# Kernel tuning notes

Measured on AMD Instinct MI355X. Metric: run time of the kernel, lower is better.

## Reference

```python
import jax, jax.numpy as jnp
import numpy as np

VOCAB = 6; C_IN = 4; D = 256; L = 4; T = 4096; B = 2
EXPAND = 2; DI = EXPAND * D  # 512
DS = 16; DCONV = 4; DTR = 16  # dt_rank = ceil(D/16)


def setup_inputs() -> dict:
    key = jax.random.key(0)
    ks = jax.random.split(key, 16)
    rn = lambda k, shape, s=0.02: jax.random.normal(k, shape, jnp.float32) * s
    return {
        "seq": jax.random.randint(ks[0], (B, T), 0, VOCAB),
        "input": jax.random.normal(ks[1], (B, T, C_IN), jnp.float32),
        "emb_table": rn(ks[2], (VOCAB, D)),
        "inproj_w": rn(ks[3], (D, C_IN)),
        "inproj_b": jnp.zeros((D,), jnp.float32),
        "blk_in_w": rn(ks[4], (L, 2 * DI, D)),
        "blk_in_b": jnp.zeros((L, 2 * DI), jnp.float32),
        "conv_w": rn(ks[5], (L, DI, DCONV), 0.1),
        "conv_b": jnp.zeros((L, DI), jnp.float32),
        "xproj_w": rn(ks[6], (L, DTR + 2 * DS, DI)),
        "dt_w": rn(ks[7], (L, DI, DTR), 0.1),
        "dt_b": rn(ks[8], (L, DI), 0.1),
        "A_log": jnp.log(jnp.broadcast_to(jnp.arange(1, DS + 1, dtype=jnp.float32), (L, DI, DS))),
        "Dp": jnp.ones((L, DI), jnp.float32),
        "blk_out_w": rn(ks[9], (L, D, DI)),
        "blk_out_b": jnp.zeros((L, D), jnp.float32),
        "ln_g": jnp.ones((L, D), jnp.float32),
        "ln_b": jnp.zeros((L, D), jnp.float32),
        "head_w": rn(ks[10], (VOCAB, D)),
        "head_b": jnp.zeros((VOCAB,), jnp.float32),
        "outp_w": rn(ks[11], (C_IN, D)),
        "outp_b": jnp.zeros((C_IN,), jnp.float32),
    }


def _layernorm(x, g, b):
    mu = x.mean(-1, keepdims=True)
    var = ((x - mu) ** 2).mean(-1, keepdims=True)
    return (x - mu) * jax.lax.rsqrt(var + 1e-5) * g + b


def _mamba(x, in_w, in_b, cw, cb, xpw, dtw, dtb, alog, dparam, ow, ob):
    # x: (B, T, D). Standard mamba-ssm Mamba block (d_state=DS, d_conv=DCONV, expand=2).
    Bsz = x.shape[0]
    xz = x @ in_w.T + in_b                      # (B, T, 2*DI)
    xs, z = jnp.split(xz, 2, axis=-1)           # each (B, T, DI)
    # causal depthwise conv1d over time
    xt = jnp.pad(xs.transpose(0, 2, 1), ((0, 0), (0, 0), (DCONV - 1, 0)))  # (B, DI, T+3)
    xc = jax.lax.conv_general_dilated(xt, cw[:, None, :], (1,), 'VALID',
                                      feature_group_count=DI)             # (B, DI, T)
    xc = jax.nn.silu(xc + cb[None, :, None]).transpose(0, 2, 1)           # (B, T, DI)
    # input-dependent dt, B, C
    x_dbl = xc @ xpw.T                          # (B, T, DTR+2*DS)
    dt, Bm, Cm = jnp.split(x_dbl, [DTR, DTR + DS], axis=-1)
    dt = jax.nn.softplus(dt @ dtw.T + dtb)      # (B, T, DI)
    A = -jnp.exp(alog)                          # (DI, DS)
    dA = jnp.exp(dt[..., None] * A)                                  # (B, T, DI, DS)
    dBx = dt[..., None] * Bm[:, :, None, :] * xc[..., None]          # (B, T, DI, DS)

    def step(h, ins):
        dA_t, dBx_t, C_t = ins                  # (B,DI,DS), (B,DI,DS), (B,DS)
        h = dA_t * h + dBx_t
        return h, jnp.einsum('bds,bs->bd', h, C_t)

    h0 = jnp.zeros((Bsz, DI, DS), xc.dtype)
    _, ys = jax.lax.scan(step, h0, (dA.transpose(1, 0, 2, 3),
                                    dBx.transpose(1, 0, 2, 3),
                                    Cm.transpose(1, 0, 2)))
    y = ys.transpose(1, 0, 2) + dparam * xc     # (B, T, DI)
    y = y * jax.nn.silu(z)
    return y @ ow.T + ob                        # (B, T, D)


def reference(seq, input, emb_table, inproj_w, inproj_b, blk_in_w, blk_in_b,
              conv_w, conv_b, xproj_w, dt_w, dt_b, A_log, Dp,
              blk_out_w, blk_out_b, ln_g, ln_b, head_w, head_b, outp_w, outp_b):
    x = emb_table[seq] + input @ inproj_w.T + inproj_b   # (B, T, D)
    for l in range(L):
        mx = _mamba(x, blk_in_w[l], blk_in_b[l], conv_w[l], conv_b[l],
                    xproj_w[l], dt_w[l], dt_b[l], A_log[l], Dp[l],
                    blk_out_w[l], blk_out_b[l])
        x = _layernorm(x + mx, ln_g[l], ln_b[l])
    return (x @ head_w.T + head_b, x @ outp_w.T + outp_b)
```

## Files before the change

kernel.cpp:

```cpp
#include <hip/hip_runtime.h>

typedef unsigned short u16;
typedef unsigned int u32;
typedef short bf16x8 __attribute__((ext_vector_type(8)));
typedef float f32x4 __attribute__((ext_vector_type(4)));

#define Tlen 4096
#define NTOK 8192
#define NCH  128
#define CH   32

enum : int {
  OFF_EMB     = 16,
  OFF_INPUT   = OFF_EMB + 1536,
  OFF_INPROJW = OFF_INPUT + 32768,
  OFF_INPROJB = OFF_INPROJW + 1024,
  OFF_BLKINW  = OFF_INPROJB + 256,
  OFF_BLKINB  = OFF_BLKINW + 1048576,
  OFF_CONVW   = OFF_BLKINB + 4096,
  OFF_CONVB   = OFF_CONVW + 8192,
  OFF_XPROJW  = OFF_CONVB + 2048,
  OFF_DTW     = OFF_XPROJW + 98304,
  OFF_DTB     = OFF_DTW + 32768,
  OFF_A       = OFF_DTB + 2048,
  OFF_DP      = OFF_A + 32768,
  OFF_BLKOUTW = OFF_DP + 2048,
  OFF_BLKOUTB = OFF_BLKOUTW + 524288,
  OFF_LNG     = OFF_BLKOUTB + 1024,
  OFF_LNB     = OFF_LNG + 1024,
  OFF_HEADW   = OFF_LNB + 1024,
  OFF_HEADB   = OFF_HEADW + 1536,
  OFF_OUTPW   = OFF_HEADB + 16,
  OFF_OUTPB   = OFF_OUTPW + 1024,
  OFF_X       = OFF_OUTPB + 16,
  OFF_DT      = OFF_X + NTOK*256,
  OFF_SD      = OFF_DT + NTOK*256,
  OFF_BM      = OFF_SD + 131072,
  OFF_CM      = OFF_BM + 131072,
  OFF_XSBL    = OFF_CM + 131072,
  OFF_Z16     = OFF_XSBL + NTOK*256,
  OFF_XC16    = OFF_Z16 + NTOK*256,
  OFF_X16     = OFF_XC16 + NTOK*256,
  OFF_WIN16   = OFF_X16 + NTOK*128,
  OFF_WOUT16  = OFF_WIN16 + 524288,
  OFF_BXD16   = OFF_WOUT16 + 262144,
  OFF_T16     = OFF_BXD16 + 49152,
  OFF_DTW16   = OFF_T16 + NTOK*16,
  OFF_TOT     = OFF_DTW16 + 32768,
};

__device__ inline float bf2f(u16 u) { return __uint_as_float(((u32)u) << 16); }
__device__ inline u16 f2bf(float f) {
  u32 x = __float_as_uint(f);
  u32 r = x + 0x7fffu + ((x >> 16) & 1u);
  return (u16)(r >> 16);
}

__global__ void k_sentinel(u32* dout, int nw) {
  int i = blockIdx.x * blockDim.x + threadIdx.x;
  if (i < nw) dout[i] = 0x46404640u;
}

__global__ void k_detect(const u16* emb, int n, int* flag) {
  __shared__ int bad;
  if (threadIdx.x == 0) bad = 0;
  __syncthreads();
  int local = 0;
  for (int i = threadIdx.x; i < n; i += blockDim.x) {
    float v = bf2f(emb[i]);
    if (!(fabsf(v) < 100.0f)) local = 1;
  }
  if (local) atomicOr(&bad, 1);
  __syncthreads();
  if (threadIdx.x == 0) flag[0] = bad ? 0 : 1;
}

struct Seg { const void* src; int n; int off; int op; };
struct ConvArgs { Seg seg[21]; int nseg; };

__global__ void k_convert(ConvArgs a, float* ws, const int* flag) {
  int isb = *flag;
  for (int sgi = 0; sgi < a.nseg; sgi++) {
    Seg sg = a.seg[sgi];
    for (int i = blockIdx.x * blockDim.x + threadIdx.x; i < sg.n;
         i += gridDim.x * blockDim.x) {
      float v;
      if (isb) v = bf2f(((const u16*)sg.src)[i]);
      else     v = ((const float*)sg.src)[i];
      if (sg.op) v = -__expf(v);
      ws[sg.off + i] = v;
    }
  }
}

__global__ void k_w16(float* ws) {
  u16* win = (u16*)(ws + OFF_WIN16);
  u16* wout = (u16*)(ws + OFF_WOUT16);
  u16* dtw16 = (u16*)(ws + OFF_DTW16);
  const int N1 = 1048576, N2 = N1 + 524288, N3 = N2 + 4 * 512 * 32;
  for (int i = blockIdx.x * blockDim.x + threadIdx.x; i < N3;
       i += gridDim.x * blockDim.x) {
    if (i < N1) {
      win[i] = f2bf(ws[OFF_BLKINW + i]);
    } else if (i < N2) {
      wout[i - N1] = f2bf(ws[OFF_BLKOUTW + i - N1]);
    } else {
      int j = i - N2;
      int l = j / (512 * 32), rem = j - l * (512 * 32);
      int row = rem >> 5, k = rem & 31;
      dtw16[j] = (k < 16) ? f2bf(ws[OFF_DTW + l * 8192 + row * 16 + k]) : 0;
    }
  }
}

__global__ void k_bxd(float* ws) {
  u16* bxd = (u16*)(ws + OFF_BXD16);
  const int NXD = 4 * 48 * 512;
  for (int idx = blockIdx.x * blockDim.x + threadIdx.x; idx < NXD;
       idx += gridDim.x * blockDim.x) {
    int l = idx / (48 * 512);
    int rem = idx - l * (48 * 512);
    int row = rem >> 9, k = rem & 511;
    const float* xpw = ws + OFF_XPROJW + l * 24576;
    float v = (row < 32) ? xpw[(16 + row) * 512 + k] : xpw[(row - 32) * 512 + k];
    bxd[idx] = f2bf(v);
  }
}

__global__ __launch_bounds__(256) void k_embed(const int* seq, float* ws) {
  int n = blockIdx.x, d = threadIdx.x;
  int s = seq[n];
  float4 iv = *(const float4*)(ws + OFF_INPUT + n * 4);
  float4 wv = *(const float4*)(ws + OFF_INPROJW + d * 4);
  float acc = ws[OFF_EMB + s * 256 + d] + ws[OFF_INPROJB + d]
            + iv.x * wv.x + iv.y * wv.y + iv.z * wv.z + iv.w * wv.w;
  ws[OFF_X + (size_t)n * 256 + d] = acc;
  ((u16*)(ws + OFF_X16))[(size_t)n * 256 + d] = f2bf(acc);
}

__global__ __launch_bounds__(256) void k_gemm_in(float* ws, int l) {
  __shared__ u16 As[128][40];
  __shared__ u16 Bs[128][40];
  __shared__ u16 ot[64][136];
  int m0 = blockIdx.x * 128, n0g = blockIdx.y * 128;
  int t = threadIdx.x;
  int w = t >> 6, lane = t & 63;
  int fr = lane & 15, fq = lane >> 4;
  int wr = (w >> 1) * 64, wc = (w & 1) * 64;
  const u16* Ab = (const u16*)(ws + OFF_X16);
  const u16* Bb = (const u16*)(ws + OFF_WIN16) + (size_t)l * 1024 * 256;
  const float* bias = ws + OFF_BLKINB + l * 1024;
  f32x4 acc[4][4] = {};
  for (int k0 = 0; k0 < 256; k0 += 32) {
    __syncthreads();
    #pragma unroll
    for (int cc = 0; cc < 2; cc++) {
      int c = t + cc * 256;
      int row = c >> 2, cg = (c & 3) * 8;
      *(uint4*)&As[row][cg] =
          *(const uint4*)(Ab + (size_t)(m0 + row) * 256 + k0 + cg);
      *(uint4*)&Bs[row][cg] =
          *(const uint4*)(Bb + (size_t)(n0g + row) * 256 + k0 + cg);
    }
    __syncthreads();
    bf16x8 af[4], bf_[4];
    #pragma unroll
    for (int f = 0; f < 4; f++) {
      af[f]  = *(const bf16x8*)&As[wr + f * 16 + fr][fq * 8];
      bf_[f] = *(const bf16x8*)&Bs[wc + f * 16 + fr][fq * 8];
    }
    #pragma unroll
    for (int i = 0; i < 4; i++)
      #pragma unroll
      for (int j = 0; j < 4; j++)
        acc[i][j] = __builtin_amdgcn_mfma_f32_16x16x32_bf16(af[i], bf_[j],
                                                            acc[i][j], 0, 0, 0);
  }
  u16* plane; int cb0;
  if (n0g < 512) { plane = (u16*)(ws + OFF_XSBL); cb0 = n0g; }
  else           { plane = (u16*)(ws + OFF_Z16);  cb0 = n0g - 512; }
  #pragma unroll
  for (int hh = 0; hh < 2; hh++) {
    __syncthreads();
    if ((w >> 1) == hh) {
      #pragma unroll
      for (int i = 0; i < 4; i++)
        #pragma unroll
        for (int j = 0; j < 4; j++) {
          int col = wc + j * 16 + fr;
          float bv = bias[n0g + col];
          #pragma unroll
          for (int r = 0; r < 4; r++)
            ot[i * 16 + fq * 4 + r][col] = f2bf(acc[i][j][r] + bv);
        }
    }
    __syncthreads();
    int row = t >> 2, c0 = (t & 3) * 32;
    uint4 q0 = *(const uint4*)&ot[row][c0];
    uint4 q1 = *(const uint4*)&ot[row][c0 + 8];
    uint4 q2 = *(const uint4*)&ot[row][c0 + 16];
    uint4 q3 = *(const uint4*)&ot[row][c0 + 24];
    u16* dst = plane + (size_t)(m0 + hh * 64 + row) * 512 + cb0 + c0;
    *(uint4*)(dst + 0) = q0;
    *(uint4*)(dst + 8) = q1;
    *(uint4*)(dst + 16) = q2;
    *(uint4*)(dst + 24) = q3;
  }
}

__global__ __launch_bounds__(512) void k_conv(float* ws, int l) {
  int n0 = blockIdx.x * 16;
  int d = threadIdx.x;
  const float* cw = ws + OFF_CONVW + l * 2048;
  float4 w4 = *(const float4*)(cw + d * 4);
  float cbv = ws[OFF_CONVB + l * 512 + d];
  const u16* xs16 = (const u16*)(ws + OFF_XSBL);
  u16* xc16 = (u16*)(ws + OFF_XC16);
  float xm3, xm2, xm1;
  if ((n0 & (Tlen - 1)) == 0) {
    xm3 = xm2 = xm1 = 0.f;
  } else {
    xm3 = bf2f(xs16[(size_t)(n0 - 3) * 512 + d]);
    xm2 = bf2f(xs16[(size_t)(n0 - 2) * 512 + d]);
    xm1 = bf2f(xs16[(size_t)(n0 - 1) * 512 + d]);
  }
  #pragma unroll
  for (int tok = 0; tok < 16; tok++) {
    int n = n0 + tok;
    float xc = bf2f(xs16[(size_t)n * 512 + d]);
    float acc = cbv + xm3 * w4.x + xm2 * w4.y + xm1 * w4.z + xc * w4.w;
    float sv = acc / (1.f + __expf(-acc));
    xc16[(size_t)n * 512 + d] = f2bf(sv);
    xm3 = xm2; xm2 = xm1; xm1 = xc;
  }
}

__global__ __launch_bounds__(256) void k_gemm_bct(float* ws, int l) {
  int m0 = blockIdx.x * 64;
  int w = threadIdx.x >> 6, lane = threadIdx.x & 63;
  const u16* Ab = (const u16*)(ws + OFF_XC16);
  const u16* Bb = (const u16*)(ws + OFF_BXD16) + (size_t)l * 48 * 512;
  int ak = (lane >> 4) * 8;
  const u16* ap = Ab + (size_t)(m0 + w * 16 + (lane & 15)) * 512 + ak;
  int rowbase = w * 16 + (lane >> 4) * 4;
  const u16* bp = Bb + (size_t)(lane & 15) * 512 + ak;
  f32x4 acc[3] = {};
  bf16x8 a0 = *(const bf16x8*)ap;
  bf16x8 b0[3];
  #pragma unroll
  for (int j = 0; j < 3; j++) b0[j] = *(const bf16x8*)(bp + (size_t)j * 8192);
  #pragma unroll 2
  for (int k0 = 1; k0 < 16; k0++) {
    bf16x8 a1 = *(const bf16x8*)(ap + k0 * 32);
    bf16x8 b1[3];
    #pragma unroll
    for (int j = 0; j < 3; j++)
      b1[j] = *(const bf16x8*)(bp + (size_t)j * 8192 + k0 * 32);
    #pragma unroll
    for (int j = 0; j < 3; j++)
      acc[j] = __builtin_amdgcn_mfma_f32_16x16x32_bf16(a0, b0[j], acc[j], 0, 0, 0);
    a0 = a1;
    #pragma unroll
    for (int j = 0; j < 3; j++) b0[j] = b1[j];
  }
  #pragma unroll
  for (int j = 0; j < 3; j++)
    acc[j] = __builtin_amdgcn_mfma_f32_16x16x32_bf16(a0, b0[j], acc[j], 0, 0, 0);
  int c = lane & 15;
  u16* t16 = (u16*)(ws + OFF_T16);
  #pragma unroll
  for (int r = 0; r < 4; r++) {
    ws[OFF_BM + (size_t)(m0 + rowbase + r) * 16 + c] = acc[0][r];
    ws[OFF_CM + (size_t)(m0 + rowbase + r) * 16 + c] = acc[1][r];
    t16[(size_t)(m0 + rowbase + r) * 32 + c] = f2bf(acc[2][r]);
    t16[(size_t)(m0 + rowbase + r) * 32 + 16 + c] = 0;
  }
}

__global__ __launch_bounds__(256) void k_dt16(float* ws, int l) {
  __shared__ u16 dts[64][136];
  int m0 = blockIdx.x * 64;
  int c0g = blockIdx.y * 64;
  int t = threadIdx.x;
  int w = t >> 6, lane = t & 63;
  int fr = lane & 15, fq = lane >> 4;
  const u16* Ab = (const u16*)(ws + OFF_T16);
  const u16* Bb = (const u16*)(ws + OFF_DTW16) + (size_t)l * 512 * 32;
  bf16x8 a = *(const bf16x8*)(Ab + (size_t)(m0 + w * 16 + fr) * 32 + fq * 8);
  f32x4 acc[4] = {};
  #pragma unroll
  for (int j = 0; j < 4; j++) {
    bf16x8 b = *(const bf16x8*)(Bb + (size_t)(c0g + j * 16 + fr) * 32 + fq * 8);
    acc[j] = __builtin_amdgcn_mfma_f32_16x16x32_bf16(a, b, acc[j], 0, 0, 0);
  }
  const float* dtb = ws + OFF_DTB + l * 512;
  int rowbase = w * 16 + fq * 4;
  #pragma unroll
  for (int j = 0; j < 4; j++) {
    float bv = dtb[c0g + j * 16 + fr];
    #pragma unroll
    for (int r = 0; r < 4; r++) {
      float s = acc[j][r] + bv;
      float dtv = (s > 20.f) ? s : log1pf(__expf(s));
      dts[rowbase + r][j * 16 + fr] = f2bf(dtv);
    }
  }
  __syncthreads();
  u16* dt16 = (u16*)(ws + OFF_DT);
  int row = t >> 2, part = t & 3;
  uint4 v0 = *(const uint4*)&dts[row][part * 16];
  uint4 v1 = *(const uint4*)&dts[row][part * 16 + 8];
  u16* dst = dt16 + (size_t)(m0 + row) * 512 + c0g + part * 16;
  *(uint4*)dst = v0;
  *(uint4*)(dst + 8) = v1;
}

__global__ __launch_bounds__(512) void k_scan1(float* ws, int l) {
  __shared__ u16 dt_s[8][512];
  __shared__ u16 xc_s[8][512];
  __shared__ float Bls[CH * 16];
  int blk = blockIdx.x;
  int b = blk >> 7, ch = blk & 127;
  int d = threadIdx.x;
  int nbase = b * Tlen + ch * CH;
  Bls[d] = ws[OFF_BM + (size_t)nbase * 16 + d];
  const float* Ap = ws + OFF_A + l * 8192 + d * 16;
  float Ar[16];
  *(float4*)&Ar[0]  = *(const float4*)(Ap + 0);
  *(float4*)&Ar[4]  = *(const float4*)(Ap + 4);
  *(float4*)&Ar[8]  = *(const float4*)(Ap + 8);
  *(float4*)&Ar[12] = *(const float4*)(Ap + 12);
  float h[16];
  #pragma unroll
  for (int s = 0; s < 16; s++) h[s] = 0.f;
  float sumdt = 0.f;
  const u16* dtg = (const u16*)(ws + OFF_DT) + (size_t)nbase * 512;
  const u16* xcg = (const u16*)(ws + OFF_XC16) + (size_t)nbase * 512;
  int lr = d >> 6, lc = (d & 63) * 8;
  uint4 pd = *(const uint4*)(dtg + (size_t)lr * 512 + lc);
  uint4 px = *(const uint4*)(xcg + (size_t)lr * 512 + lc);
  for (int st = 0; st < 4; st++) {
    *(uint4*)&dt_s[lr][lc] = pd;
    *(uint4*)&xc_s[lr][lc] = px;
    if (st < 3) {
      pd = *(const uint4*)(dtg + (size_t)(st * 8 + 8 + lr) * 512 + lc);
      px = *(const uint4*)(xcg + (size_t)(st * 8 + 8 + lr) * 512 + lc);
    }
    __syncthreads();
    #pragma unroll
    for (int tk = 0; tk < 8; tk++) {
      int tt = st * 8 + tk;
      float dtv = bf2f(dt_s[tk][d]);
      float xv = bf2f(xc_s[tk][d]);
      sumdt += dtv;
      float dtx = dtv * xv;
      #pragma unroll
      for (int s = 0; s < 16; s++)
        h[s] = __expf(dtv * Ar[s]) * h[s] + dtx * Bls[tt * 16 + s];
    }
    __syncthreads();
  }
  ws[OFF_SD + (size_t)blk * 512 + d] = sumdt;
  float* bl = ws + OFF_XSBL + ((size_t)blk * 512 + d) * 16;
  *(float4*)(bl + 0)  = make_float4(h[0], h[1], h[2], h[3]);
  *(float4*)(bl + 4)  = make_float4(h[4], h[5], h[6], h[7]);
  *(float4*)(bl + 8)  = make_float4(h[8], h[9], h[10], h[11]);
  *(float4*)(bl + 12) = make_float4(h[12], h[13], h[14], h[15]);
}

__global__ __launch_bounds__(256) void k_scan2(float* ws, int l) {
  int q = blockIdx.x * 256 + threadIdx.x;
  int b = q >> 13, ds = q & 8191, d = ds >> 4;
  float Av = ws[OFF_A + l * 8192 + ds];
  float* blhs = ws + OFF_XSBL;
  const float* sdp = ws + OFF_SD;
  size_t base = (size_t)(b * NCH) * 8192 + ds;
  size_t sbase = (size_t)(b * NCH) * 512 + d;
  float blv[4], sd[4];
  #pragma unroll
  for (int k = 0; k < 4; k++) {
    blv[k] = blhs[base + (size_t)k * 8192];
    sd[k] = sdp[sbase + (size_t)k * 512];
  }
  float h = 0.f;
  for (int g = 0; g < 32; g++) {
    float nblv[4], nsd[4];
    if (g < 31) {
      #pragma unroll
      for (int k = 0; k < 4; k++) {
        nblv[k] = blhs[base + (size_t)(g * 4 + 4 + k) * 8192];
        nsd[k] = sdp[sbase + (size_t)(g * 4 + 4 + k) * 512];
      }
    }
    #pragma unroll
    for (int k = 0; k < 4; k++) {
      blhs[base + (size_t)(g * 4 + k) * 8192] = h;
      h = __expf(sd[k] * Av) * h + blv[k];
    }
    #pragma unroll
    for (int k = 0; k < 4; k++) { blv[k] = nblv[k]; sd[k] = nsd[k]; }
  }
}

__global__ __launch_bounds__(512) void k_scan3(float* ws, int l) {
  __shared__ u16 dt_s[8][512];
  __shared__ u16 xc_s[8][512];
  __shared__ u16 z_s[8][512];
  __shared__ u16 y_s[8][512];
  __shared__ float Bls[CH * 16];
  __shared__ float Cls[CH * 16];
  int blk = blockIdx.x;
  int b = blk >> 7, ch = blk & 127;
  int d = threadIdx.x;
  int nbase = b * Tlen + ch * CH;
  Bls[d] = ws[OFF_BM + (size_t)nbase * 16 + d];
  Cls[d] = ws[OFF_CM + (size_t)nbase * 16 + d];
  const float* Ap = ws + OFF_A + l * 8192 + d * 16;
  float Ar[16];
  *(float4*)&Ar[0]  = *(const float4*)(Ap + 0);
  *(float4*)&Ar[4]  = *(const float4*)(Ap + 4);
  *(float4*)&Ar[8]  = *(const float4*)(Ap + 8);
  *(float4*)&Ar[12] = *(const float4*)(Ap + 12);
  float Dv = ws[OFF_DP + l * 512 + d];
  const float* hs = ws + OFF_XSBL + ((size_t)blk * 512 + d) * 16;
  float h[16];
  *(float4*)&h[0]  = *(const float4*)(hs + 0);
  *(float4*)&h[4]  = *(const float4*)(hs + 4);
  *(float4*)&h[8]  = *(const float4*)(hs + 8);
  *(float4*)&h[12] = *(const float4*)(hs + 12);
  const u16* dtg = (const u16*)(ws + OFF_DT) + (size_t)nbase * 512;
  u16* xcg = (u16*)(ws + OFF_XC16) + (size_t)nbase * 512;
  const u16* zg = (const u16*)(ws + OFF_Z16) + (size_t)nbase * 512;
  int lr = d >> 6, lc = (d & 63) * 8;
  size_t off0 = (size_t)lr * 512 + lc;
  uint4 pd = *(const uint4*)(dtg + off0);
  uint4 px = *(const uint4*)(xcg + off0);
  uint4 pz = *(const uint4*)(zg + off0);
  for (int st = 0; st < 4; st++) {
    size_t goff = (size_t)(st * 8 + lr) * 512 + lc;
    *(uint4*)&dt_s[lr][lc] = pd;
    *(uint4*)&xc_s[lr][lc] = px;
    *(uint4*)&z_s[lr][lc]  = pz;
    if (st < 3) {
      size_t noff = (size_t)(st * 8 + 8 + lr) * 512 + lc;
      pd = *(const uint4*)(dtg + noff);
      px = *(const uint4*)(xcg + noff);
      pz = *(const uint4*)(zg + noff);
    }
    __syncthreads();
    #pragma unroll
    for (int tk = 0; tk < 8; tk++) {
      int tt = st * 8 + tk;
      float dtv = bf2f(dt_s[tk][d]);
      float xv = bf2f(xc_s[tk][d]);
      float dtx = dtv * xv;
      float yacc = 0.f;
      #pragma unroll
      for (int s = 0; s < 16; s++) {
        h[s] = __expf(dtv * Ar[s]) * h[s] + dtx * Bls[tt * 16 + s];
        yacc += h[s] * Cls[tt * 16 + s];
      }
      float yv = yacc + Dv * xv;
      float zv = bf2f(z_s[tk][d]);
      float sz = zv / (1.f + __expf(-zv));
      y_s[tk][d] = f2bf(yv * sz);
    }
    __syncthreads();
    *(uint4*)(xcg + goff) = *(const uint4*)&y_s[lr][lc];
  }
}

__global__ __launch_bounds__(256) void k_gemm_out(float* ws, int l) {
  __shared__ float mxs[16][260];
  int m0 = blockIdx.x * 16;
  int w = threadIdx.x >> 6, lane = threadIdx.x & 63;
  const u16* Ab = (const u16*)(ws + OFF_XC16);
  const u16* Bb = (const u16*)(ws + OFF_WOUT16) + (size_t)l * 256 * 512;
  int ak = (lane >> 4) * 8;
  const u16* ap = Ab + (size_t)(m0 + (lane & 15)) * 512 + ak;
  const u16* bp = Bb + (size_t)(w * 64 + (lane & 15)) * 512 + ak;
  f32x4 acc[4] = {};
  bf16x8 a0 = *(const bf16x8*)ap;
  bf16x8 b0[4];
  #pragma unroll
  for (int j = 0; j < 4; j++) b0[j] = *(const bf16x8*)(bp + (size_t)j * 8192);
  #pragma unroll 2
  for (int k0 = 1; k0 < 16; k0++) {
    bf16x8 a1 = *(const bf16x8*)(ap + k0 * 32);
    bf16x8 b1[4];
    #pragma unroll
    for (int j = 0; j < 4; j++)
      b1[j] = *(const bf16x8*)(bp + (size_t)j * 8192 + k0 * 32);
    #pragma unroll
    for (int j = 0; j < 4; j++)
      acc[j] = __builtin_amdgcn_mfma_f32_16x16x32_bf16(a0, b0[j], acc[j], 0, 0, 0);
    a0 = a1;
    #pragma unroll
    for (int j = 0; j < 4; j++) b0[j] = b1[j];
  }
  #pragma unroll
  for (int j = 0; j < 4; j++)
    acc[j] = __builtin_amdgcn_mfma_f32_16x16x32_bf16(a0, b0[j], acc[j], 0, 0, 0);
  const float* ob = ws + OFF_BLKOUTB + l * 256;
  int rl = (lane >> 4) * 4;
  #pragma unroll
  for (int j = 0; j < 4; j++) {
    int c = w * 64 + j * 16 + (lane & 15);
    float bv = ob[c];
    #pragma unroll
    for (int r = 0; r < 4; r++)
      mxs[rl + r][c] = acc[j][r] + bv;
  }
  __syncthreads();
  int t = threadIdx.x;
  int g = t >> 4, ln = t & 15;
  int n = m0 + g;
  float* x = ws + OFF_X;
  const float* gamma = ws + OFF_LNG + l * 256;
  const float* beta = ws + OFF_LNB + l * 256;
  float v[16], s1 = 0.f, s2 = 0.f;
  #pragma unroll
  for (int i = 0; i < 16; i++) {
    int c = ln + i * 16;
    float xv = x[(size_t)n * 256 + c] + mxs[g][c];
    v[i] = xv; s1 += xv; s2 += xv * xv;
  }
  #pragma unroll
  for (int m = 8; m >= 1; m >>= 1) {
    s1 += __shfl_xor(s1, m, 64);
    s2 += __shfl_xor(s2, m, 64);
  }
  float mu = s1 * (1.f / 256.f);
  float var = s2 * (1.f / 256.f) - mu * mu;
  float rs = rsqrtf(var + 1e-5f);
  #pragma unroll
  for (int i = 0; i < 16; i++) {
    int c = ln + i * 16;
    mxs[g][c] = (v[i] - mu) * rs * gamma[c] + beta[c];
  }
  __syncthreads();
  int row = t >> 4, cb = (t & 15) * 16;
  float4 f0 = *(const float4*)&mxs[row][cb + 0];
  float4 f1 = *(const float4*)&mxs[row][cb + 4];
  float4 f2 = *(const float4*)&mxs[row][cb + 8];
  float4 f3 = *(const float4*)&mxs[row][cb + 12];
  float* xd = x + (size_t)(m0 + row) * 256 + cb;
  *(float4*)(xd + 0) = f0;
  *(float4*)(xd + 4) = f1;
  *(float4*)(xd + 8) = f2;
  *(float4*)(xd + 12) = f3;
  u32 p[8];
  p[0] = (u32)f2bf(f0.x) | ((u32)f2bf(f0.y) << 16);
  p[1] = (u32)f2bf(f0.z) | ((u32)f2bf(f0.w) << 16);
  p[2] = (u32)f2bf(f1.x) | ((u32)f2bf(f1.y) << 16);
  p[3] = (u32)f2bf(f1.z) | ((u32)f2bf(f1.w) << 16);
  p[4] = (u32)f2bf(f2.x) | ((u32)f2bf(f2.y) << 16);
  p[5] = (u32)f2bf(f2.z) | ((u32)f2bf(f2.w) << 16);
  p[6] = (u32)f2bf(f3.x) | ((u32)f2bf(f3.y) << 16);
  p[7] = (u32)f2bf(f3.z) | ((u32)f2bf(f3.w) << 16);
  u16* xd16 = (u16*)(ws + OFF_X16) + (size_t)(m0 + row) * 256 + cb;
  *(uint4*)(xd16 + 0) = *(uint4*)&p[0];
  *(uint4*)(xd16 + 8) = *(uint4*)&p[4];
}

__global__ __launch_bounds__(256) void k_head(const float* ws, void* dout,
                                              const int* flag) {
  int t = threadIdx.x;
  int lane = t & 63, w = t >> 6;
  int n = blockIdx.x * 4 + w;
  const float* xr = ws + OFF_X + (size_t)n * 256;
  float xv[4];
  #pragma unroll
  for (int i = 0; i < 4; i++) xv[i] = xr[lane + 64 * i];
  float res[10];
  #pragma unroll
  for (int o = 0; o < 10; o++) {
    const float* wr = (o < 6) ? ws + OFF_HEADW + o * 256
                              : ws + OFF_OUTPW + (o - 6) * 256;
    float p = 0.f;
    #pragma unroll
    for (int i = 0; i < 4; i++) p += xv[i] * wr[lane + 64 * i];
    #pragma unroll
    for (int m = 32; m >= 1; m >>= 1) p += __shfl_xor(p, m, 64);
    res[o] = p;
  }
  int isb = flag[0];
  if (lane < 6) {
    float vv = res[lane] + ws[OFF_HEADB + lane];
    size_t idx = (size_t)n * 6 + lane;
    if (isb) ((u16*)dout)[idx] = f2bf(vv);
    else     ((float*)dout)[idx] = vv;
  } else if (lane < 10) {
    int o = lane - 6;
    float vv = res[lane] + ws[OFF_OUTPB + o];
    size_t idx = (size_t)NTOK * 6 + (size_t)n * 4 + o;
    if (isb) ((u16*)dout)[idx] = f2bf(vv);
    else     ((float*)dout)[idx] = vv;
  }
}

extern "C" void kernel_launch(void* const* d_in, const int* in_sizes, int n_in,
                              void* d_out, int out_size, void* d_ws, size_t ws_size,
                              hipStream_t stream) {
  (void)n_in;
  float* ws = (float*)d_ws;
  int* flag = (int*)d_ws;

  if (ws_size < (size_t)OFF_TOT * 4) {
    int nw = out_size / 2;
    k_sentinel<<<(nw + 255) / 256, 256, 0, stream>>>((u32*)d_out, nw);
    return;
  }

  k_detect<<<1, 256, 0, stream>>>((const u16*)d_in[2], in_sizes[2], flag);

  ConvArgs ca;
  int i = 0;
  auto add = [&](int idx, int n, int off, int op) {
    ca.seg[i].src = d_in[idx]; ca.seg[i].n = n;
    ca.seg[i].off = off; ca.seg[i].op = op; i++;
  };
  add(2, 1536, OFF_EMB, 0);      add(1, 32768, OFF_INPUT, 0);
  add(3, 1024, OFF_INPROJW, 0);  add(4, 256, OFF_INPROJB, 0);
  add(5, 1048576, OFF_BLKINW, 0); add(6, 4096, OFF_BLKINB, 0);
  add(7, 8192, OFF_CONVW, 0);    add(8, 2048, OFF_CONVB, 0);
  add(9, 98304, OFF_XPROJW, 0);  add(10, 32768, OFF_DTW, 0);
  add(11, 2048, OFF_DTB, 0);     add(12, 32768, OFF_A, 1);
  add(13, 2048, OFF_DP, 0);      add(14, 524288, OFF_BLKOUTW, 0);
  add(15, 1024, OFF_BLKOUTB, 0); add(16, 1024, OFF_LNG, 0);
  add(17, 1024, OFF_LNB, 0);     add(18, 1536, OFF_HEADW, 0);
  add(19, 6, OFF_HEADB, 0);      add(20, 1024, OFF_OUTPW, 0);
  add(21, 4, OFF_OUTPB, 0);
  ca.nseg = i;
  k_convert<<<512, 256, 0, stream>>>(ca, ws, flag);
  k_w16<<<512, 256, 0, stream>>>(ws);
  k_bxd<<<384, 256, 0, stream>>>(ws);

  k_embed<<<NTOK, 256, 0, stream>>>((const int*)d_in[0], ws);

  for (int l = 0; l < 4; l++) {
    k_gemm_in<<<dim3(64, 8), 256, 0, stream>>>(ws, l);
    k_conv<<<NTOK / 16, 512, 0, stream>>>(ws, l);
    k_gemm_bct<<<128, 256, 0, stream>>>(ws, l);
    k_dt16<<<dim3(128, 8), 256, 0, stream>>>(ws, l);
    k_scan1<<<2 * NCH, 512, 0, stream>>>(ws, l);
    k_scan2<<<64, 256, 0, stream>>>(ws, l);
    k_scan3<<<2 * NCH, 512, 0, stream>>>(ws, l);
    k_gemm_out<<<NTOK / 16, 256, 0, stream>>>(ws, l);
  }

  k_head<<<NTOK / 4, 256, 0, stream>>>(ws, d_out, flag);
}
```

Baseline: 550.3 us.

## Halve scan chunk length and store inter-chunk states as bf16

```diff
diff --git a/kernel.cpp b/kernel.cpp
--- a/kernel.cpp
+++ b/kernel.cpp
@@ -7,8 +7,8 @@
 
 #define Tlen 4096
 #define NTOK 8192
-#define NCH  128
-#define CH   32
+#define NCH  256
+#define CH   16
 
 enum : int {
   OFF_EMB     = 16,
@@ -35,7 +35,7 @@
   OFF_X       = OFF_OUTPB + 16,
   OFF_DT      = OFF_X + NTOK*256,
   OFF_SD      = OFF_DT + NTOK*256,
-  OFF_BM      = OFF_SD + 131072,
+  OFF_BM      = OFF_SD + 262144,
   OFF_CM      = OFF_BM + 131072,
   OFF_XSBL    = OFF_CM + 131072,
   OFF_Z16     = OFF_XSBL + NTOK*256,
@@ -54,6 +54,9 @@
   u32 x = __float_as_uint(f);
   u32 r = x + 0x7fffu + ((x >> 16) & 1u);
   return (u16)(r >> 16);
+}
+__device__ inline u32 pk2(float a, float b) {
+  return (u32)f2bf(a) | ((u32)f2bf(b) << 16);
 }
 
 __global__ void k_sentinel(u32* dout, int nw) {
@@ -320,10 +323,10 @@
   __shared__ u16 xc_s[8][512];
   __shared__ float Bls[CH * 16];
   int blk = blockIdx.x;
-  int b = blk >> 7, ch = blk & 127;
+  int b = blk >> 8, ch = blk & 255;
   int d = threadIdx.x;
   int nbase = b * Tlen + ch * CH;
-  Bls[d] = ws[OFF_BM + (size_t)nbase * 16 + d];
+  if (d < CH * 16) Bls[d] = ws[OFF_BM + (size_t)nbase * 16 + d];
   const float* Ap = ws + OFF_A + l * 8192 + d * 16;
   float Ar[16];
   *(float4*)&Ar[0]  = *(const float4*)(Ap + 0);
@@ -339,12 +342,12 @@
   int lr = d >> 6, lc = (d & 63) * 8;
   uint4 pd = *(const uint4*)(dtg + (size_t)lr * 512 + lc);
   uint4 px = *(const uint4*)(xcg + (size_t)lr * 512 + lc);
-  for (int st = 0; st < 4; st++) {
+  for (int st = 0; st < 2; st++) {
     *(uint4*)&dt_s[lr][lc] = pd;
     *(uint4*)&xc_s[lr][lc] = px;
-    if (st < 3) {
-      pd = *(const uint4*)(dtg + (size_t)(st * 8 + 8 + lr) * 512 + lc);
-      px = *(const uint4*)(xcg + (size_t)(st * 8 + 8 + lr) * 512 + lc);
+    if (st < 1) {
+      pd = *(const uint4*)(dtg + (size_t)(8 + lr) * 512 + lc);
+      px = *(const uint4*)(xcg + (size_t)(8 + lr) * 512 + lc);
     }
     __syncthreads();
     #pragma unroll
@@ -361,40 +364,41 @@
     __syncthreads();
   }
   ws[OFF_SD + (size_t)blk * 512 + d] = sumdt;
-  float* bl = ws + OFF_XSBL + ((size_t)blk * 512 + d) * 16;
-  *(float4*)(bl + 0)  = make_float4(h[0], h[1], h[2], h[3]);
-  *(float4*)(bl + 4)  = make_float4(h[4], h[5], h[6], h[7]);
-  *(float4*)(bl + 8)  = make_float4(h[8], h[9], h[10], h[11]);
-  *(float4*)(bl + 12) = make_float4(h[12], h[13], h[14], h[15]);
+  u16* bl = (u16*)(ws + OFF_XSBL) + ((size_t)blk * 512 + d) * 16;
+  u32 pk[8];
+  #pragma unroll
+  for (int i = 0; i < 8; i++) pk[i] = pk2(h[2 * i], h[2 * i + 1]);
+  *(uint4*)(bl + 0) = *(uint4*)&pk[0];
+  *(uint4*)(bl + 8) = *(uint4*)&pk[4];
 }
 
 __global__ __launch_bounds__(256) void k_scan2(float* ws, int l) {
   int q = blockIdx.x * 256 + threadIdx.x;
   int b = q >> 13, ds = q & 8191, d = ds >> 4;
   float Av = ws[OFF_A + l * 8192 + ds];
-  float* blhs = ws + OFF_XSBL;
+  u16* blhs = (u16*)(ws + OFF_XSBL);
   const float* sdp = ws + OFF_SD;
   size_t base = (size_t)(b * NCH) * 8192 + ds;
   size_t sbase = (size_t)(b * NCH) * 512 + d;
   float blv[4], sd[4];
   #pragma unroll
   for (int k = 0; k < 4; k++) {
-    blv[k] = blhs[base + (size_t)k * 8192];
+    blv[k] = bf2f(blhs[base + (size_t)k * 8192]);
     sd[k] = sdp[sbase + (size_t)k * 512];
   }
   float h = 0.f;
-  for (int g = 0; g < 32; g++) {
+  for (int g = 0; g < NCH / 4; g++) {
     float nblv[4], nsd[4];
-    if (g < 31) {
+    if (g < NCH / 4 - 1) {
       #pragma unroll
       for (int k = 0; k < 4; k++) {
-        nblv[k] = blhs[base + (size_t)(g * 4 + 4 + k) * 8192];
+        nblv[k] = bf2f(blhs[base + (size_t)(g * 4 + 4 + k) * 8192]);
         nsd[k] = sdp[sbase + (size_t)(g * 4 + 4 + k) * 512];
       }
     }
     #pragma unroll
     for (int k = 0; k < 4; k++) {
-      blhs[base + (size_t)(g * 4 + k) * 8192] = h;
+      blhs[base + (size_t)(g * 4 + k) * 8192] = f2bf(h);
       h = __expf(sd[k] * Av) * h + blv[k];
     }
     #pragma unroll
@@ -410,11 +414,13 @@
   __shared__ float Bls[CH * 16];
   __shared__ float Cls[CH * 16];
   int blk = blockIdx.x;
-  int b = blk >> 7, ch = blk & 127;
+  int b = blk >> 8, ch = blk & 255;
   int d = threadIdx.x;
   int nbase = b * Tlen + ch * CH;
-  Bls[d] = ws[OFF_BM + (size_t)nbase * 16 + d];
-  Cls[d] = ws[OFF_CM + (size_t)nbase * 16 + d];
+  if (d < CH * 16) {
+    Bls[d] = ws[OFF_BM + (size_t)nbase * 16 + d];
+    Cls[d] = ws[OFF_CM + (size_t)nbase * 16 + d];
+  }
   const float* Ap = ws + OFF_A + l * 8192 + d * 16;
   float Ar[16];
   *(float4*)&Ar[0]  = *(const float4*)(Ap + 0);
@@ -422,12 +428,24 @@
   *(float4*)&Ar[8]  = *(const float4*)(Ap + 8);
   *(float4*)&Ar[12] = *(const float4*)(Ap + 12);
   float Dv = ws[OFF_DP + l * 512 + d];
-  const float* hs = ws + OFF_XSBL + ((size_t)blk * 512 + d) * 16;
+  const u16* hsp = (const u16*)(ws + OFF_XSBL) + ((size_t)blk * 512 + d) * 16;
+  uint4 hq0 = *(const uint4*)(hsp + 0);
+  uint4 hq1 = *(const uint4*)(hsp + 8);
   float h[16];
-  *(float4*)&h[0]  = *(const float4*)(hs + 0);
-  *(float4*)&h[4]  = *(const float4*)(hs + 4);
-  *(float4*)&h[8]  = *(const float4*)(hs + 8);
-  *(float4*)&h[12] = *(const float4*)(hs + 12);
+  {
+    const u32* hw = (const u32*)&hq0;
+    #pragma unroll
+    for (int i = 0; i < 4; i++) {
+      h[2 * i] = bf2f((u16)hw[i]);
+      h[2 * i + 1] = bf2f((u16)(hw[i] >> 16));
+    }
+    const u32* hw1 = (const u32*)&hq1;
+    #pragma unroll
+    for (int i = 0; i < 4; i++) {
+      h[8 + 2 * i] = bf2f((u16)hw1[i]);
+      h[8 + 2 * i + 1] = bf2f((u16)(hw1[i] >> 16));
+    }
+  }
   const u16* dtg = (const u16*)(ws + OFF_DT) + (size_t)nbase * 512;
   u16* xcg = (u16*)(ws + OFF_XC16) + (size_t)nbase * 512;
   const u16* zg = (const u16*)(ws + OFF_Z16) + (size_t)nbase * 512;
@@ -436,13 +454,13 @@
   uint4 pd = *(const uint4*)(dtg + off0);
   uint4 px = *(const uint4*)(xcg + off0);
   uint4 pz = *(const uint4*)(zg + off0);
-  for (int st = 0; st < 4; st++) {
+  for (int st = 0; st < 2; st++) {
     size_t goff = (size_t)(st * 8 + lr) * 512 + lc;
     *(uint4*)&dt_s[lr][lc] = pd;
     *(uint4*)&xc_s[lr][lc] = px;
     *(uint4*)&z_s[lr][lc]  = pz;
-    if (st < 3) {
-      size_t noff = (size_t)(st * 8 + 8 + lr) * 512 + lc;
+    if (st < 1) {
+      size_t noff = (size_t)(8 + lr) * 512 + lc;
       pd = *(const uint4*)(dtg + noff);
       px = *(const uint4*)(xcg + noff);
       pz = *(const uint4*)(zg + noff);
@@ -550,14 +568,14 @@
   *(float4*)(xd + 8) = f2;
   *(float4*)(xd + 12) = f3;
   u32 p[8];
-  p[0] = (u32)f2bf(f0.x) | ((u32)f2bf(f0.y) << 16);
-  p[1] = (u32)f2bf(f0.z) | ((u32)f2bf(f0.w) << 16);
-  p[2] = (u32)f2bf(f1.x) | ((u32)f2bf(f1.y) << 16);
-  p[3] = (u32)f2bf(f1.z) | ((u32)f2bf(f1.w) << 16);
-  p[4] = (u32)f2bf(f2.x) | ((u32)f2bf(f2.y) << 16);
-  p[5] = (u32)f2bf(f2.z) | ((u32)f2bf(f2.w) << 16);
-  p[6] = (u32)f2bf(f3.x) | ((u32)f2bf(f3.y) << 16);
-  p[7] = (u32)f2bf(f3.z) | ((u32)f2bf(f3.w) << 16);
+  p[0] = pk2(f0.x, f0.y);
+  p[1] = pk2(f0.z, f0.w);
+  p[2] = pk2(f1.x, f1.y);
+  p[3] = pk2(f1.z, f1.w);
+  p[4] = pk2(f2.x, f2.y);
+  p[5] = pk2(f2.z, f2.w);
+  p[6] = pk2(f3.x, f3.y);
+  p[7] = pk2(f3.z, f3.w);
   u16* xd16 = (u16*)(ws + OFF_X16) + (size_t)(m0 + row) * 256 + cb;
   *(uint4*)(xd16 + 0) = *(uint4*)&p[0];
   *(uint4*)(xd16 + 8) = *(uint4*)&p[4];
```

After: 587.3 us. +6.7%, slower.
